# Performance work log

Measured on AMD Instinct MI355X. Metric: run time of the kernel, lower is better.

The kernel has to match this reference:

```python
import jax, jax.numpy as jnp
import numpy as np

# Dims chosen per init_kwargs / input_specs
LEVELS = 2      # data_in_levels (residual binarization depth)
K = 4           # data_in_k (LUT fan-in)
KK = 2 ** K     # LUT table size
IN = 128        # in_features
OUT = 128       # out_features
BATCH = 128
T = IN * OUT    # tables_count = mask_builder.get_tables_count() * out_features


def setup_inputs() -> dict:
    key = jax.random.key(0)
    k1, k2, k3, k4 = jax.random.split(key, 4)
    x = jax.random.normal(k1, (BATCH, IN), dtype=jnp.float32)
    # trainer weight: one 2^k-entry LUT per table
    weight = jax.random.normal(k2, (T, KK), dtype=jnp.float32) * 0.1
    bias = jax.random.normal(k3, (OUT,), dtype=jnp.float32) * 0.1
    # means init: ars = levels..1 (reversed arange+1), normalized
    ars = (np.arange(LEVELS) + 1.0)[::-1]
    means = jnp.asarray(ars / ars.sum(), dtype=jnp.float32)
    # MaskExpanded: per (out_feature, in_feature) table of k input indices;
    # first index is the table's own in_idx, the rest drawn from the others.
    rnd = jax.random.randint(k4, (OUT, IN, K), 0, IN)
    first = jnp.broadcast_to(jnp.arange(IN)[None, :, None], (OUT, IN, 1))
    input_mask = jnp.concatenate([first, rnd[..., 1:]], axis=-1).reshape(-1).astype(jnp.int32)
    return {"x": x, "weight": weight, "bias": bias, "means": means, "input_mask": input_mask}


def _truth_table():
    # all 2^k bipolar codes in {-1,+1}^k, shape [KK, K]
    codes = (jnp.arange(KK)[:, None] >> jnp.arange(K)[None, :]) & 1
    return (2 * codes - 1).astype(jnp.float32)


def residual_sign(x, means):
    # ReBNet residual sign quantizer: level-l output is +-|means[l]|, residual updated
    resid = x
    outs = []
    for l in range(LEVELS):
        s = jnp.where(resid >= 0, 1.0, -1.0)  # bipolar binary_quantizer
        o = jnp.abs(means[l]) * s
        outs.append(o)
        resid = resid - o
    return jnp.stack(outs)  # [LEVELS, B, IN]


def reference(x, weight, bias, means, input_mask):
    B = x.shape[0]
    out_bin = residual_sign(x, means)                   # [L, B, IN]
    expanded = out_bin[:, :, input_mask]                # irregular gather -> [L, B, T*K]
    xk = expanded.reshape(LEVELS, B, T, K)              # per-table k inputs
    tt = _truth_table()                                 # [KK, K]
    # Lagrange basis on {-1,+1}^k: prod_i (1 + x_i * c_i) / 2  -> [L, B, T, KK]
    basis = jnp.prod((1.0 + xk[..., None, :] * tt) * 0.5, axis=-1)
    # LUT eval (contract KK) and sum over residual levels -> [B, T]
    table_out = jnp.einsum('lbtc,tc->bt', basis, weight)
    # grouped segment-sum: each output feature sums its in_features tables
    out = table_out.reshape(B, OUT, IN).sum(-1) + bias  # [B, OUT]
    return out
```

## Files before the change

### kernel.cpp

```cpp
#include <hip/hip_runtime.h>
#include <stdint.h>

#define IN_    128
#define OUT_   128
#define BATCH_ 128
#define KK_    16
#define BPB    32
#define SBSTRIDE 36

__global__ __launch_bounds__(256) void linlut_kernel(
    const float* __restrict__ x, const float* __restrict__ w,
    const float* __restrict__ bias, const float* __restrict__ means,
    const int* __restrict__ mask, float* __restrict__ out)
{
    __shared__ float         lut[128 * 33];
    __shared__ unsigned char sbT[IN_ * SBSTRIDE];
    __shared__ uint32_t      pidx[128];
    __shared__ float         partial[8 * 33];

    const int tid = threadIdx.x;
    const int o  = blockIdx.x >> 2;
    const int b0 = (blockIdx.x & 3) * BPB;

    const float m0 = fabsf(means[0]);
    const float m1 = fabsf(means[1]);
    const float bo = bias[o];

    if (tid < 128) {
        const int4 mm = *(const int4*)(mask + ((size_t)(o * IN_ + tid)) * 4);
        pidx[tid] = (uint32_t)mm.x | ((uint32_t)mm.y << 8) |
                    ((uint32_t)mm.z << 16) | ((uint32_t)mm.w << 24);
    }

    #pragma unroll
    for (int r = 0; r < 4; ++r) {
        const int item = tid + 256 * r;
        const int b    = item >> 5;
        const int g    = item & 31;
        const float4 xv = *(const float4*)(x + (size_t)(b0 + b) * IN_ + g * 4);
        const float vv[4] = {xv.x, xv.y, xv.z, xv.w};
        #pragma unroll
        for (int k = 0; k < 4; ++k) {
            const uint32_t s0 = (vv[k] >= 0.0f) ? 1u : 0u;
            const float rr = vv[k] - (s0 ? m0 : -m0);
            const uint32_t s1 = (rr >= 0.0f) ? 1u : 0u;
            sbT[(4 * g + k) * SBSTRIDE + b] = (unsigned char)(s0 | (s1 << 1));
        }
    }

    {
        const int i   = tid >> 1;
        const int lvl = tid & 1;
        const float m = lvl ? m1 : m0;
        const float p = (1.0f + m) * 0.5f;
        const float q = (1.0f - m) * 0.5f;
        float pw[5];
        pw[0] = p * p * p * p;
        pw[1] = p * p * p * q;
        pw[2] = p * p * q * q;
        pw[3] = p * q * q * q;
        pw[4] = q * q * q * q;
        const float* wr = w + ((size_t)(o * IN_ + i)) * KK_;
        float wv[16];
        #pragma unroll
        for (int c4 = 0; c4 < 4; ++c4) {
            const float4 t = *(const float4*)(wr + 4 * c4);
            wv[4 * c4 + 0] = t.x; wv[4 * c4 + 1] = t.y;
            wv[4 * c4 + 2] = t.z; wv[4 * c4 + 3] = t.w;
        }
        float* lr = lut + i * 33 + lvl * 16;
        #pragma unroll
        for (int S = 0; S < 16; ++S) {
            float acc = 0.0f;
            #pragma unroll
            for (int c = 0; c < 16; ++c)
                acc += wv[c] * pw[__popc(S ^ c)];
            lr[S] = acc;
        }
    }
    __syncthreads();

    const int bcol = tid & 31;
    const int part = tid >> 5;
    const unsigned char* sb = sbT + bcol;
    float acc = 0.0f;
    #pragma unroll
    for (int j = 0; j < 16; ++j) {
        const int i = part * 16 + j;
        const uint32_t pk = pidx[i];
        const uint32_t c0 = sb[(pk & 255u) * SBSTRIDE];
        const uint32_t c1 = sb[((pk >> 8) & 255u) * SBSTRIDE];
        const uint32_t c2 = sb[((pk >> 16) & 255u) * SBSTRIDE];
        const uint32_t c3 = sb[(pk >> 24) * SBSTRIDE];
        const uint32_t S0 = (c0 & 1u) | ((c1 & 1u) << 1) | ((c2 & 1u) << 2) | ((c3 & 1u) << 3);
        const uint32_t S1 = (c0 >> 1) | ((c1 >> 1) << 1) | ((c2 >> 1) << 2) | ((c3 >> 1) << 3);
        const float* lr = lut + i * 33;
        acc += lr[S0];
        acc += lr[16 + S1];
    }
    partial[part * 33 + bcol] = acc;
    __syncthreads();

    if (tid < 32) {
        float s = 0.0f;
        #pragma unroll
        for (int p = 0; p < 8; ++p)
            s += partial[p * 33 + tid];
        out[(size_t)(b0 + tid) * OUT_ + o] = s + bo;
    }
}

extern "C" void kernel_launch(void* const* d_in, const int* in_sizes, int n_in,
                              void* d_out, int out_size, void* d_ws, size_t ws_size,
                              hipStream_t stream) {
    const float* x     = (const float*)d_in[0];
    const float* w     = (const float*)d_in[1];
    const float* bias  = (const float*)d_in[2];
    const float* means = (const float*)d_in[3];
    const int*   mask  = (const int*)d_in[4];
    float* out = (float*)d_out;
    hipLaunchKernelGGL(linlut_kernel, dim3(512), dim3(256), 0, stream,
                       x, w, bias, means, mask, out);
}
```

Before: 65.03 us.

## Split batch finer, compute LUT via Walsh-Hadamard transforms, shuffle-reduce partials

Batch per block drops from 32 to 8, so the grid grows to 2048 blocks, and block IDs are swizzled to spread output features across XCDs. The LUT precompute replaces the 16x16 popcount-weighted sum with forward and inverse Walsh-Hadamard butterflies plus a diagonal scaling. Global loads are issued up front, and the cross-part reduction uses wavefront shuffles instead of a shared partial array. Each block still rebuilds the full 128-table LUT, so per-batch LUT work rises fourfold while each block's gather loop gets shorter.

```diff
diff --git a/kernel.cpp b/kernel.cpp
--- a/kernel.cpp
+++ b/kernel.cpp
@@ -3,109 +3,115 @@
 
 #define IN_    128
 #define OUT_   128
-#define BATCH_ 128
 #define KK_    16
-#define BPB    32
-#define SBSTRIDE 36
+#define BPB    8
+#define SSTR   9
 
-__global__ __launch_bounds__(256) void linlut_kernel(
+__global__ __launch_bounds__(256, 8) void linlut_kernel(
     const float* __restrict__ x, const float* __restrict__ w,
     const float* __restrict__ bias, const float* __restrict__ means,
     const int* __restrict__ mask, float* __restrict__ out)
 {
     __shared__ float         lut[128 * 33];
-    __shared__ unsigned char sbT[IN_ * SBSTRIDE];
+    __shared__ unsigned char sbT[IN_ * SSTR];
     __shared__ uint32_t      pidx[128];
-    __shared__ float         partial[8 * 33];
+    __shared__ float         wpart[4][8];
 
     const int tid = threadIdx.x;
-    const int o  = blockIdx.x >> 2;
-    const int b0 = (blockIdx.x & 3) * BPB;
+    const uint32_t bid = blockIdx.x;
+    const uint32_t L   = (bid & 7u) * 256u + (bid >> 3);
+    const int o  = (int)(L >> 4);
+    const int b0 = (int)(L & 15u) * BPB;
+
+    const int i3  = tid >> 1;
+    const int lvl = tid & 1;
+    const float4* wr = (const float4*)(w + ((size_t)(o * IN_ + i3)) * KK_);
+    const float4 w0 = wr[0], w1 = wr[1], w2 = wr[2], w3 = wr[3];
+
+    const int xb = tid >> 5, xg = tid & 31;
+    const float4 xv = *(const float4*)(x + (size_t)(b0 + xb) * IN_ + xg * 4);
+
+    int4 mm = make_int4(0, 0, 0, 0);
+    if (tid < 128) mm = *(const int4*)(mask + ((size_t)(o * IN_ + tid)) * 4);
 
     const float m0 = fabsf(means[0]);
     const float m1 = fabsf(means[1]);
     const float bo = bias[o];
 
-    if (tid < 128) {
-        const int4 mm = *(const int4*)(mask + ((size_t)(o * IN_ + tid)) * 4);
+    if (tid < 128)
         pidx[tid] = (uint32_t)mm.x | ((uint32_t)mm.y << 8) |
                     ((uint32_t)mm.z << 16) | ((uint32_t)mm.w << 24);
-    }
 
-    #pragma unroll
-    for (int r = 0; r < 4; ++r) {
-        const int item = tid + 256 * r;
-        const int b    = item >> 5;
-        const int g    = item & 31;
-        const float4 xv = *(const float4*)(x + (size_t)(b0 + b) * IN_ + g * 4);
+    {
         const float vv[4] = {xv.x, xv.y, xv.z, xv.w};
         #pragma unroll
         for (int k = 0; k < 4; ++k) {
             const uint32_t s0 = (vv[k] >= 0.0f) ? 1u : 0u;
-            const float rr = vv[k] - (s0 ? m0 : -m0);
-            const uint32_t s1 = (rr >= 0.0f) ? 1u : 0u;
-            sbT[(4 * g + k) * SBSTRIDE + b] = (unsigned char)(s0 | (s1 << 1));
+            const float r = vv[k] - (s0 ? m0 : -m0);
+            const uint32_t s1 = (r >= 0.0f) ? 1u : 0u;
+            sbT[(4 * xg + k) * SSTR + xb] = (unsigned char)(s0 | (s1 << 1));
         }
     }
 
     {
-        const int i   = tid >> 1;
-        const int lvl = tid & 1;
         const float m = lvl ? m1 : m0;
-        const float p = (1.0f + m) * 0.5f;
-        const float q = (1.0f - m) * 0.5f;
-        float pw[5];
-        pw[0] = p * p * p * p;
-        pw[1] = p * p * p * q;
-        pw[2] = p * p * q * q;
-        pw[3] = p * q * q * q;
-        pw[4] = q * q * q * q;
-        const float* wr = w + ((size_t)(o * IN_ + i)) * KK_;
-        float wv[16];
+        float v[16] = {w0.x, w0.y, w0.z, w0.w, w1.x, w1.y, w1.z, w1.w,
+                       w2.x, w2.y, w2.z, w2.w, w3.x, w3.y, w3.z, w3.w};
         #pragma unroll
-        for (int c4 = 0; c4 < 4; ++c4) {
-            const float4 t = *(const float4*)(wr + 4 * c4);
-            wv[4 * c4 + 0] = t.x; wv[4 * c4 + 1] = t.y;
-            wv[4 * c4 + 2] = t.z; wv[4 * c4 + 3] = t.w;
-        }
-        float* lr = lut + i * 33 + lvl * 16;
+        for (int s = 1; s < 16; s <<= 1)
+            #pragma unroll
+            for (int a = 0; a < 16; ++a)
+                if ((a & s) == 0) {
+                    const float u = v[a], t2 = v[a | s];
+                    v[a] = u + t2; v[a | s] = u - t2;
+                }
+        const float c0 = 0.0625f;
+        const float c1 = m * c0, c2 = m * c1, c3 = m * c2, c4 = m * c3;
+        v[0]  *= c0;
+        v[1]  *= c1; v[2]  *= c1; v[4]  *= c1; v[8]  *= c1;
+        v[3]  *= c2; v[5]  *= c2; v[6]  *= c2; v[9]  *= c2; v[10] *= c2; v[12] *= c2;
+        v[7]  *= c3; v[11] *= c3; v[13] *= c3; v[14] *= c3;
+        v[15] *= c4;
         #pragma unroll
-        for (int S = 0; S < 16; ++S) {
-            float acc = 0.0f;
+        for (int s = 1; s < 16; s <<= 1)
             #pragma unroll
-            for (int c = 0; c < 16; ++c)
-                acc += wv[c] * pw[__popc(S ^ c)];
-            lr[S] = acc;
-        }
+            for (int a = 0; a < 16; ++a)
+                if ((a & s) == 0) {
+                    const float u = v[a], t2 = v[a | s];
+                    v[a] = u + t2; v[a | s] = u - t2;
+                }
+        float* lr = lut + i3 * 33 + lvl * 16;
+        #pragma unroll
+        for (int S = 0; S < 16; ++S) lr[S] = v[S];
     }
     __syncthreads();
 
-    const int bcol = tid & 31;
-    const int part = tid >> 5;
+    const int part = tid >> 3;
+    const int bcol = tid & 7;
     const unsigned char* sb = sbT + bcol;
     float acc = 0.0f;
     #pragma unroll
-    for (int j = 0; j < 16; ++j) {
-        const int i = part * 16 + j;
+    for (int j = 0; j < 4; ++j) {
+        const int i = part * 4 + j;
         const uint32_t pk = pidx[i];
-        const uint32_t c0 = sb[(pk & 255u) * SBSTRIDE];
-        const uint32_t c1 = sb[((pk >> 8) & 255u) * SBSTRIDE];
-        const uint32_t c2 = sb[((pk >> 16) & 255u) * SBSTRIDE];
-        const uint32_t c3 = sb[(pk >> 24) * SBSTRIDE];
-        const uint32_t S0 = (c0 & 1u) | ((c1 & 1u) << 1) | ((c2 & 1u) << 2) | ((c3 & 1u) << 3);
-        const uint32_t S1 = (c0 >> 1) | ((c1 >> 1) << 1) | ((c2 >> 1) << 2) | ((c3 >> 1) << 3);
+        const uint32_t cc0 = sb[(pk & 255u) * SSTR];
+        const uint32_t cc1 = sb[((pk >> 8) & 255u) * SSTR];
+        const uint32_t cc2 = sb[((pk >> 16) & 255u) * SSTR];
+        const uint32_t cc3 = sb[(pk >> 24) * SSTR];
+        const uint32_t S0 = (cc0 & 1u) | ((cc1 & 1u) << 1) | ((cc2 & 1u) << 2) | ((cc3 & 1u) << 3);
+        const uint32_t S1 = (cc0 >> 1) | ((cc1 >> 1) << 1) | ((cc2 >> 1) << 2) | ((cc3 >> 1) << 3);
         const float* lr = lut + i * 33;
         acc += lr[S0];
         acc += lr[16 + S1];
     }
-    partial[part * 33 + bcol] = acc;
+    acc += __shfl_xor(acc, 8);
+    acc += __shfl_xor(acc, 16);
+    acc += __shfl_xor(acc, 32);
+    if ((tid & 63) < 8) wpart[tid >> 6][bcol] = acc;
     __syncthreads();
 
-    if (tid < 32) {
-        float s = 0.0f;
-        #pragma unroll
-        for (int p = 0; p < 8; ++p)
-            s += partial[p * 33 + tid];
+    if (tid < 8) {
+        const float s = wpart[0][tid] + wpart[1][tid] + wpart[2][tid] + wpart[3][tid];
         out[(size_t)(b0 + tid) * OUT_ + o] = s + bo;
     }
 }
@@ -119,6 +125,6 @@
     const float* means = (const float*)d_in[3];
     const int*   mask  = (const int*)d_in[4];
     float* out = (float*)d_out;
-    hipLaunchKernelGGL(linlut_kernel, dim3(512), dim3(256), 0, stream,
+    hipLaunchKernelGGL(linlut_kernel, dim3(2048), dim3(256), 0, stream,
                        x, w, bias, means, mask, out);
 }
```

Measured after the change: 66.57 us. 2.4% more time.
